# Kernel tuning notes

Hardware: AMD Instinct MI355X
Metric: run time of the kernel (lower is better)

The kernel has to match this reference:

```python
import jax, jax.numpy as jnp
import numpy as np

B, TQ, TP, DQ, DP = 16, 1024, 1024, 1024, 1024

def setup_inputs() -> dict:
    key = jax.random.key(0)
    kq, kp, kw = jax.random.split(key, 3)
    q = jax.random.normal(kq, (B, TQ, DQ), dtype=jnp.float32)
    p = jax.random.normal(kp, (B, TP, DP), dtype=jnp.float32)
    W = jax.random.normal(kw, (DP, DQ), dtype=jnp.float32) / np.sqrt(DP)
    return {"q": q, "p": p, "W": W}

def reference(q, p, W):
    # pW: [B, Tp, Dq]
    pW = jnp.einsum('bpe,ed->bpd', p, W)
    # bilinear scores: [B, Tp, Tq]
    scores = jnp.einsum('bpd,bqd->bpq', pW, q)
    # NOTE: original softmaxes over axis=-2 of [B, Tp, Tq] == the Tp axis
    weights = jax.nn.softmax(scores, axis=1)
    # weighted sum over Tq: [B, Tp, Dq]
    out = jnp.einsum('bpq,bqd->bpd', weights, q)
    return out
```

## Files before the change

kernel.cpp:

```cpp
#include <hip/hip_runtime.h>
#include <cstddef>
#include <cstdint>


namespace {

using u16 = unsigned short;
using frag  = __attribute__((ext_vector_type(8))) short;
using f32x4 = __attribute__((ext_vector_type(4))) float;

constexpr int kB = 16;
constexpr int kT = 1024;
constexpr int kD = 1024;
constexpr int BM = 128, BN = 128, BK = 32;
constexpr int KSTEPS = kD / BK;

union FragU { frag v; u16 u[8]; };

__device__ __forceinline__ u16 f2bf(float x) {
  uint32_t u = __float_as_uint(x);
  return (u16)((u + 0x7FFFu + ((u >> 16) & 1u)) >> 16);
}
__device__ __forceinline__ float bf2f(u16 h) {
  return __uint_as_float(((uint32_t)h) << 16);
}

#define AS1(p) (const __attribute__((address_space(1))) void*)(p)
#define AS3(p) (__attribute__((address_space(3))) void*)(p)

__device__ __forceinline__ void gl_lds16(const u16* g, u16* l) {
  __builtin_amdgcn_global_load_lds(AS1(g), AS3(l), 16, 0, 0);
}

__device__ __forceinline__ void stage_glds(const u16* __restrict__ src, u16* lds,
                                           int row0, int k0, int tid) {
  const int w = tid >> 6, l = tid & 63;
#pragma unroll
  for (int rr = 0; rr < 2; ++rr) {
    const int chunk = rr * 4 + w;
    const int row = chunk * 16 + (l >> 2);
    const int kc = (l & 3) * 8;
    gl_lds16(src + (size_t)(row0 + row) * 1024 + k0 + kc, lds + chunk * 512);
  }
}

struct Reg16 { float4 v[4]; };

__device__ __forceinline__ Reg16 load_tile16(const float* __restrict__ src,
                                             int row0, int k0, int tid) {
  const int r = tid >> 1, c0 = (tid & 1) << 4;
  const float4* g = (const float4*)(src + (size_t)(row0 + r) * 1024 + k0 + c0);
  Reg16 out;
#pragma unroll
  for (int i = 0; i < 4; ++i) out.v[i] = g[i];
  return out;
}

__device__ __forceinline__ void write_split(const Reg16& rg, u16* ldsHi, u16* ldsLo,
                                            int tid) {
  const int r = tid >> 1, c0 = (tid & 1) << 4;
  float vv[16];
#pragma unroll
  for (int i = 0; i < 4; ++i) {
    vv[4*i+0] = rg.v[i].x; vv[4*i+1] = rg.v[i].y;
    vv[4*i+2] = rg.v[i].z; vv[4*i+3] = rg.v[i].w;
  }
  FragU h0, l0, h1, l1;
#pragma unroll
  for (int i = 0; i < 8; ++i) {
    u16 h = f2bf(vv[i]);     h0.u[i] = h; l0.u[i] = f2bf(vv[i]     - bf2f(h));
  }
#pragma unroll
  for (int i = 0; i < 8; ++i) {
    u16 h = f2bf(vv[8+i]);   h1.u[i] = h; l1.u[i] = f2bf(vv[8+i]   - bf2f(h));
  }
  *(frag*)(ldsHi + r*32 + c0)     = h0.v;
  *(frag*)(ldsHi + r*32 + c0 + 8) = h1.v;
  *(frag*)(ldsLo + r*32 + c0)     = l0.v;
  *(frag*)(ldsLo + r*32 + c0 + 8) = l1.v;
}

__device__ __forceinline__ void write_split_exp(const Reg16& rg, const float* mL,
                                                const float* rL, u16* ldsHi,
                                                u16* ldsLo, int k0, int tid) {
  const int r = tid >> 1, c0 = (tid & 1) << 4;
  float vv[16];
#pragma unroll
  for (int i = 0; i < 4; ++i) {
    vv[4*i+0] = rg.v[i].x; vv[4*i+1] = rg.v[i].y;
    vv[4*i+2] = rg.v[i].z; vv[4*i+3] = rg.v[i].w;
  }
#pragma unroll
  for (int i = 0; i < 16; ++i) {
    const int k = k0 + c0 + i;
    vv[i] = __expf(vv[i] - mL[k]) * rL[k];
  }
  FragU h0, l0, h1, l1;
#pragma unroll
  for (int i = 0; i < 8; ++i) {
    u16 h = f2bf(vv[i]);   h0.u[i] = h; l0.u[i] = f2bf(vv[i]   - bf2f(h));
  }
#pragma unroll
  for (int i = 0; i < 8; ++i) {
    u16 h = f2bf(vv[8+i]); h1.u[i] = h; l1.u[i] = f2bf(vv[8+i] - bf2f(h));
  }
  *(frag*)(ldsHi + r*32 + c0)     = h0.v;
  *(frag*)(ldsHi + r*32 + c0 + 8) = h1.v;
  *(frag*)(ldsLo + r*32 + c0)     = l0.v;
  *(frag*)(ldsLo + r*32 + c0 + 8) = l1.v;
}

__device__ __forceinline__ void compute_step(const u16* AhS, const u16* AlS,
                                             const u16* BhS, const u16* BlS,
                                             f32x4 acc[4][4], int lane, int wr, int wc) {
  const int kb = (lane >> 4) * 8;
  const int ra = lane & 15;
  frag ah[4], al[4];
#pragma unroll
  for (int m = 0; m < 4; ++m) {
    const int row = wr*64 + m*16 + ra;
    ah[m] = *(const frag*)(AhS + row*32 + kb);
    al[m] = *(const frag*)(AlS + row*32 + kb);
  }
#pragma unroll
  for (int n = 0; n < 4; ++n) {
    const int col = wc*64 + n*16 + ra;
    const frag bh = *(const frag*)(BhS + col*32 + kb);
    const frag bl = *(const frag*)(BlS + col*32 + kb);
#pragma unroll
    for (int m = 0; m < 4; ++m) {
      acc[m][n] = __builtin_amdgcn_mfma_f32_16x16x32_bf16(ah[m], bh, acc[m][n], 0, 0, 0);
      acc[m][n] = __builtin_amdgcn_mfma_f32_16x16x32_bf16(al[m], bh, acc[m][n], 0, 0, 0);
      acc[m][n] = __builtin_amdgcn_mfma_f32_16x16x32_bf16(ah[m], bl, acc[m][n], 0, 0, 0);
    }
  }
}

__device__ __forceinline__ void epilogue_f32(float* __restrict__ dst, f32x4 acc[4][4],
                                             int row0, int col0, int lane, int wr, int wc) {
#pragma unroll
  for (int m = 0; m < 4; ++m)
#pragma unroll
    for (int n = 0; n < 4; ++n) {
      const int col = col0 + wc*64 + n*16 + (lane & 15);
      const int rb  = row0 + wr*64 + m*16 + ((lane >> 4) << 2);
#pragma unroll
      for (int j = 0; j < 4; ++j)
        dst[(size_t)(rb + j) * 1024 + col] = acc[m][n][j];
    }
}

__global__ __launch_bounds__(256) void g1_pw(const float* __restrict__ P,
                                             const u16* __restrict__ WTh,
                                             const u16* __restrict__ WTl,
                                             u16* __restrict__ pWh,
                                             u16* __restrict__ pWl) {
  __shared__ u16 AhS[BM*BK], AlS[BM*BK], BhS[BN*BK], BlS[BN*BK];
  const int tid = threadIdx.x, lane = tid & 63;
  const int wid = tid >> 6, wr = wid >> 1, wc = wid & 1;
  const int m0 = blockIdx.y * BM, n0 = blockIdx.x * BN;

  f32x4 acc[4][4];
#pragma unroll
  for (int m = 0; m < 4; ++m)
#pragma unroll
    for (int n = 0; n < 4; ++n) acc[m][n] = (f32x4){0.f, 0.f, 0.f, 0.f};

  Reg16 a = load_tile16(P, m0, 0, tid);
#pragma unroll 1
  for (int ks = 0; ks < KSTEPS; ++ks) {
    const int k0 = ks * BK;
    __syncthreads();
    stage_glds(WTh, BhS, n0, k0, tid);
    stage_glds(WTl, BlS, n0, k0, tid);
    write_split(a, AhS, AlS, tid);
    if (ks + 1 < KSTEPS) a = load_tile16(P, m0, k0 + BK, tid);
    __syncthreads();
    compute_step(AhS, AlS, BhS, BlS, acc, lane, wr, wc);
  }

#pragma unroll
  for (int m = 0; m < 4; ++m)
#pragma unroll
    for (int n = 0; n < 4; ++n) {
      const int col = n0 + wc*64 + n*16 + (lane & 15);
      const int rb  = m0 + wr*64 + m*16 + ((lane >> 4) << 2);
#pragma unroll
      for (int j = 0; j < 4; ++j) {
        const float x = acc[m][n][j];
        const u16 h = f2bf(x);
        pWh[(size_t)(rb + j) * 1024 + col] = h;
        pWl[(size_t)(rb + j) * 1024 + col] = f2bf(x - bf2f(h));
      }
    }
}

__global__ __launch_bounds__(256) void g2_scores(const u16* __restrict__ pWh,
                                                 const u16* __restrict__ pWl,
                                                 const float* __restrict__ Q,
                                                 float* __restrict__ S) {
  __shared__ u16 AhS[BM*BK], AlS[BM*BK], BhS[BN*BK], BlS[BN*BK];
  const int tid = threadIdx.x, lane = tid & 63;
  const int wid = tid >> 6, wr = wid >> 1, wc = wid & 1;
  const int b = blockIdx.z;
  const int m0 = blockIdx.y * BM, n0 = blockIdx.x * BN;
  const int rowA0 = b * kT + m0;
  const float* Qb = Q + (size_t)b * kT * kD;
  float* Sb = S + (size_t)b * kT * kT;

  f32x4 acc[4][4];
#pragma unroll
  for (int m = 0; m < 4; ++m)
#pragma unroll
    for (int n = 0; n < 4; ++n) acc[m][n] = (f32x4){0.f, 0.f, 0.f, 0.f};

  Reg16 bq = load_tile16(Qb, n0, 0, tid);
#pragma unroll 1
  for (int ks = 0; ks < KSTEPS; ++ks) {
    const int k0 = ks * BK;
    __syncthreads();
    stage_glds(pWh, AhS, rowA0, k0, tid);
    stage_glds(pWl, AlS, rowA0, k0, tid);
    write_split(bq, BhS, BlS, tid);
    if (ks + 1 < KSTEPS) bq = load_tile16(Qb, n0, k0 + BK, tid);
    __syncthreads();
    compute_step(AhS, AlS, BhS, BlS, acc, lane, wr, wc);
  }
  epilogue_f32(Sb, acc, m0, n0, lane, wr, wc);
}

__global__ __launch_bounds__(256) void k3_stats(const float* __restrict__ S,
                                                float* __restrict__ mOut,
                                                float* __restrict__ rlOut) {
  const int b = blockIdx.y;
  const int q0 = blockIdx.x * 32;
  const int t = threadIdx.x;
  const int c = t & 31, g = t >> 5;
  const float* Sb = S + (size_t)b * kT * kT + q0 + c;

  float m = -3.4e38f, l = 0.f;
#pragma unroll 4
  for (int p = g; p < kT; p += 8) {
    const float x = Sb[(size_t)p * kT];
    if (x <= m) {
      l += __expf(x - m);
    } else {
      l = l * __expf(m - x) + 1.f;
      m = x;
    }
  }
  __shared__ float sm[8][32], sl[8][32];
  sm[g][c] = m;
  sl[g][c] = l;
  __syncthreads();
  if (t < 32) {
    float M = sm[0][t];
#pragma unroll
    for (int g2 = 1; g2 < 8; ++g2) M = fmaxf(M, sm[g2][t]);
    float L = 0.f;
#pragma unroll
    for (int g2 = 0; g2 < 8; ++g2) L += sl[g2][t] * __expf(sm[g2][t] - M);
    mOut[(size_t)b * kT + q0 + t] = M;
    rlOut[(size_t)b * kT + q0 + t] = 1.f / L;
  }
}

__global__ __launch_bounds__(256) void conv_t_split(const float* __restrict__ src,
                                                    u16* __restrict__ dstH,
                                                    u16* __restrict__ dstL) {
  __shared__ float ts[64][65];
  const size_t boff = (size_t)blockIdx.z * kT * kD;
  const int t = threadIdx.x;
  const int i0 = blockIdx.y * 64, j0 = blockIdx.x * 64;
  const int r = t >> 2, c0 = (t & 3) << 4;
  const float4* g = (const float4*)(src + boff + (size_t)(i0 + r) * 1024 + j0 + c0);
#pragma unroll
  for (int i = 0; i < 4; ++i) {
    const float4 v = g[i];
    ts[r][c0 + 4*i + 0] = v.x; ts[r][c0 + 4*i + 1] = v.y;
    ts[r][c0 + 4*i + 2] = v.z; ts[r][c0 + 4*i + 3] = v.w;
  }
  __syncthreads();
  FragU h0, l0, h1, l1;
#pragma unroll
  for (int i = 0; i < 8; ++i) {
    const float x = ts[c0 + i][r];
    const u16 h = f2bf(x); h0.u[i] = h; l0.u[i] = f2bf(x - bf2f(h));
  }
#pragma unroll
  for (int i = 0; i < 8; ++i) {
    const float x = ts[c0 + 8 + i][r];
    const u16 h = f2bf(x); h1.u[i] = h; l1.u[i] = f2bf(x - bf2f(h));
  }
  u16* dh = dstH + boff + (size_t)(j0 + r) * 1024 + i0 + c0;
  u16* dl = dstL + boff + (size_t)(j0 + r) * 1024 + i0 + c0;
  *(frag*)dh = h0.v; *((frag*)dh + 1) = h1.v;
  *(frag*)dl = l0.v; *((frag*)dl + 1) = l1.v;
}

__global__ __launch_bounds__(256) void g4_out(const float* __restrict__ S,
                                              const float* __restrict__ mArr,
                                              const float* __restrict__ rlArr,
                                              const u16* __restrict__ qTh,
                                              const u16* __restrict__ qTl,
                                              float* __restrict__ Out) {
  __shared__ u16 AhS[BM*BK], AlS[BM*BK], BhS[BN*BK], BlS[BN*BK];
  __shared__ float mL[kT], rL[kT];
  const int tid = threadIdx.x, lane = tid & 63;
  const int wid = tid >> 6, wr = wid >> 1, wc = wid & 1;
  const int b = blockIdx.z;
  const int m0 = blockIdx.y * BM, n0 = blockIdx.x * BN;
  const float* Sb = S + (size_t)b * kT * kT;
  const u16* qThb = qTh + (size_t)b * kT * kD;
  const u16* qTlb = qTl + (size_t)b * kT * kD;
  float* Ob = Out + (size_t)b * kT * kD;

  for (int i = tid; i < kT; i += 256) {
    mL[i] = mArr[(size_t)b * kT + i];
    rL[i] = rlArr[(size_t)b * kT + i];
  }

  f32x4 acc[4][4];
#pragma unroll
  for (int m = 0; m < 4; ++m)
#pragma unroll
    for (int n = 0; n < 4; ++n) acc[m][n] = (f32x4){0.f, 0.f, 0.f, 0.f};

  Reg16 a = load_tile16(Sb, m0, 0, tid);
#pragma unroll 1
  for (int ks = 0; ks < KSTEPS; ++ks) {
    const int k0 = ks * BK;
    __syncthreads();
    stage_glds(qThb, BhS, n0, k0, tid);
    stage_glds(qTlb, BlS, n0, k0, tid);
    write_split_exp(a, mL, rL, AhS, AlS, k0, tid);
    if (ks + 1 < KSTEPS) a = load_tile16(Sb, m0, k0 + BK, tid);
    __syncthreads();
    compute_step(AhS, AlS, BhS, BlS, acc, lane, wr, wc);
  }
  epilogue_f32(Ob, acc, m0, n0, lane, wr, wc);
}

}

extern "C" void kernel_launch(void* const* d_in, const int* in_sizes, int n_in,
                              void* d_out, int out_size, void* d_ws, size_t ws_size,
                              hipStream_t stream) {
  const float* q = (const float*)d_in[0];
  const float* p = (const float*)d_in[1];
  const float* W = (const float*)d_in[2];
  float* out = (float*)d_out;

  char* wsb = (char*)d_ws;
  u16* pWh = (u16*)wsb;
  u16* pWl = (u16*)(wsb + (32ull << 20));
  u16* qTh = pWh;
  u16* qTl = pWl;
  float* S   = (float*)(wsb + (64ull << 20));
  u16* WTh = (u16*)(wsb + (64ull << 20));
  u16* WTl = (u16*)(wsb + (64ull << 20) + (2ull << 20));
  float* mArr  = (float*)(wsb + (128ull << 20));
  float* rlArr = mArr + (size_t)kB * kT;

  const dim3 blk(256);
  conv_t_split<<<dim3(16, 16, 1), blk, 0, stream>>>(W, WTh, WTl);
  g1_pw<<<dim3(kD / BN, (kB * kT) / BM), blk, 0, stream>>>(p, WTh, WTl, pWh, pWl);
  g2_scores<<<dim3(kT / BN, kT / BM, kB), blk, 0, stream>>>(pWh, pWl, q, S);
  k3_stats<<<dim3(kT / 32, kB), blk, 0, stream>>>(S, mArr, rlArr);
  conv_t_split<<<dim3(16, 16, kB), blk, 0, stream>>>(q, qTh, qTl);
  g4_out<<<dim3(kD / BN, kT / BM, kB), blk, 0, stream>>>(S, mArr, rlArr, qTh, qTl, out);
}
```

Measured before the change: 613.3 us.

## Store scores transposed, precompute split-bf16 softmax weights, fragment-ordered LDS tiles

Scores are now computed as [q,p] so the softmax over p becomes a contiguous row reduction done by one wave per row. A new kernel applies exp and normalization, transposes the result and writes split-bf16 weights, so the final GEMM stages both operands directly with global-to-LDS loads instead of converting fp32 in registers. LDS tiles switch to an MFMA fragment-ordered layout so each lane reads contiguous 16 bytes. This adds an extra full pass over the score matrix and more workspace traffic in exchange for cheaper strided reductions and simpler GEMM inner loops.

```diff
diff --git a/kernel.cpp b/kernel.cpp
--- a/kernel.cpp
+++ b/kernel.cpp
@@ -32,101 +32,65 @@
   __builtin_amdgcn_global_load_lds(AS1(g), AS3(l), 16, 0, 0);
 }
 
-__device__ __forceinline__ void stage_glds(const u16* __restrict__ src, u16* lds,
-                                           int row0, int k0, int tid) {
+
+__device__ __forceinline__ void stage_frag_glds(const u16* __restrict__ src,
+                                                u16* lds, int row0, int k0, int tid) {
   const int w = tid >> 6, l = tid & 63;
-#pragma unroll
-  for (int rr = 0; rr < 2; ++rr) {
-    const int chunk = rr * 4 + w;
-    const int row = chunk * 16 + (l >> 2);
-    const int kc = (l & 3) * 8;
-    gl_lds16(src + (size_t)(row0 + row) * 1024 + k0 + kc, lds + chunk * 512);
-  }
-}
-
-struct Reg16 { float4 v[4]; };
-
-__device__ __forceinline__ Reg16 load_tile16(const float* __restrict__ src,
-                                             int row0, int k0, int tid) {
-  const int r = tid >> 1, c0 = (tid & 1) << 4;
-  const float4* g = (const float4*)(src + (size_t)(row0 + r) * 1024 + k0 + c0);
-  Reg16 out;
-#pragma unroll
-  for (int i = 0; i < 4; ++i) out.v[i] = g[i];
-  return out;
-}
-
-__device__ __forceinline__ void write_split(const Reg16& rg, u16* ldsHi, u16* ldsLo,
-                                            int tid) {
-  const int r = tid >> 1, c0 = (tid & 1) << 4;
-  float vv[16];
-#pragma unroll
-  for (int i = 0; i < 4; ++i) {
-    vv[4*i+0] = rg.v[i].x; vv[4*i+1] = rg.v[i].y;
-    vv[4*i+2] = rg.v[i].z; vv[4*i+3] = rg.v[i].w;
-  }
-  FragU h0, l0, h1, l1;
-#pragma unroll
-  for (int i = 0; i < 8; ++i) {
-    u16 h = f2bf(vv[i]);     h0.u[i] = h; l0.u[i] = f2bf(vv[i]     - bf2f(h));
-  }
-#pragma unroll
-  for (int i = 0; i < 8; ++i) {
-    u16 h = f2bf(vv[8+i]);   h1.u[i] = h; l1.u[i] = f2bf(vv[8+i]   - bf2f(h));
-  }
-  *(frag*)(ldsHi + r*32 + c0)     = h0.v;
-  *(frag*)(ldsHi + r*32 + c0 + 8) = h1.v;
-  *(frag*)(ldsLo + r*32 + c0)     = l0.v;
-  *(frag*)(ldsLo + r*32 + c0 + 8) = l1.v;
-}
-
-__device__ __forceinline__ void write_split_exp(const Reg16& rg, const float* mL,
-                                                const float* rL, u16* ldsHi,
-                                                u16* ldsLo, int k0, int tid) {
-  const int r = tid >> 1, c0 = (tid & 1) << 4;
-  float vv[16];
-#pragma unroll
-  for (int i = 0; i < 4; ++i) {
-    vv[4*i+0] = rg.v[i].x; vv[4*i+1] = rg.v[i].y;
-    vv[4*i+2] = rg.v[i].z; vv[4*i+3] = rg.v[i].w;
-  }
-#pragma unroll
-  for (int i = 0; i < 16; ++i) {
-    const int k = k0 + c0 + i;
-    vv[i] = __expf(vv[i] - mL[k]) * rL[k];
-  }
-  FragU h0, l0, h1, l1;
-#pragma unroll
-  for (int i = 0; i < 8; ++i) {
-    u16 h = f2bf(vv[i]);   h0.u[i] = h; l0.u[i] = f2bf(vv[i]   - bf2f(h));
-  }
-#pragma unroll
-  for (int i = 0; i < 8; ++i) {
-    u16 h = f2bf(vv[8+i]); h1.u[i] = h; l1.u[i] = f2bf(vv[8+i] - bf2f(h));
-  }
-  *(frag*)(ldsHi + r*32 + c0)     = h0.v;
-  *(frag*)(ldsHi + r*32 + c0 + 8) = h1.v;
-  *(frag*)(ldsLo + r*32 + c0)     = l0.v;
-  *(frag*)(ldsLo + r*32 + c0 + 8) = l1.v;
+  const int rl = l & 15;
+  const int kc = (l >> 4) * 8;
+#pragma unroll
+  for (int i = 0; i < 2; ++i) {
+    const int g = w * 2 + i;
+    gl_lds16(src + (size_t)(row0 + g * 16 + rl) * 1024 + k0 + kc, lds + g * 512);
+  }
+}
+
+__device__ __forceinline__ void load_f32_slots(const float* __restrict__ src,
+                                               int row0, int k0, int tid, float4* out) {
+#pragma unroll
+  for (int i = 0; i < 2; ++i) {
+    const int s = tid + i * 256;
+    const int row = (s >> 6) * 16 + (s & 15);
+    const int kc = ((s >> 4) & 3) * 8;
+    const float4* g = (const float4*)(src + (size_t)(row0 + row) * 1024 + k0 + kc);
+    out[i * 2 + 0] = g[0];
+    out[i * 2 + 1] = g[1];
+  }
+}
+
+__device__ __forceinline__ void write_split_frag(const float4* v, u16* ldsHi,
+                                                 u16* ldsLo, int tid) {
+#pragma unroll
+  for (int i = 0; i < 2; ++i) {
+    const int s = tid + i * 256;
+    const float vv[8] = {v[2*i].x, v[2*i].y, v[2*i].z, v[2*i].w,
+                         v[2*i+1].x, v[2*i+1].y, v[2*i+1].z, v[2*i+1].w};
+    FragU h, lo;
+#pragma unroll
+    for (int j = 0; j < 8; ++j) {
+      const u16 hh = f2bf(vv[j]);
+      h.u[j] = hh;
+      lo.u[j] = f2bf(vv[j] - bf2f(hh));
+    }
+    *(frag*)(ldsHi + s * 8) = h.v;
+    *(frag*)(ldsLo + s * 8) = lo.v;
+  }
 }
 
 __device__ __forceinline__ void compute_step(const u16* AhS, const u16* AlS,
                                              const u16* BhS, const u16* BlS,
                                              f32x4 acc[4][4], int lane, int wr, int wc) {
-  const int kb = (lane >> 4) * 8;
-  const int ra = lane & 15;
+  const int lo16 = lane * 8;
   frag ah[4], al[4];
 #pragma unroll
   for (int m = 0; m < 4; ++m) {
-    const int row = wr*64 + m*16 + ra;
-    ah[m] = *(const frag*)(AhS + row*32 + kb);
-    al[m] = *(const frag*)(AlS + row*32 + kb);
+    ah[m] = *(const frag*)(AhS + (wr * 4 + m) * 512 + lo16);
+    al[m] = *(const frag*)(AlS + (wr * 4 + m) * 512 + lo16);
   }
 #pragma unroll
   for (int n = 0; n < 4; ++n) {
-    const int col = wc*64 + n*16 + ra;
-    const frag bh = *(const frag*)(BhS + col*32 + kb);
-    const frag bl = *(const frag*)(BlS + col*32 + kb);
+    const frag bh = *(const frag*)(BhS + (wc * 4 + n) * 512 + lo16);
+    const frag bl = *(const frag*)(BlS + (wc * 4 + n) * 512 + lo16);
 #pragma unroll
     for (int m = 0; m < 4; ++m) {
       acc[m][n] = __builtin_amdgcn_mfma_f32_16x16x32_bf16(ah[m], bh, acc[m][n], 0, 0, 0);
@@ -142,8 +106,8 @@
   for (int m = 0; m < 4; ++m)
 #pragma unroll
     for (int n = 0; n < 4; ++n) {
-      const int col = col0 + wc*64 + n*16 + (lane & 15);
-      const int rb  = row0 + wr*64 + m*16 + ((lane >> 4) << 2);
+      const int col = col0 + wc * 64 + n * 16 + (lane & 15);
+      const int rb  = row0 + wr * 64 + m * 16 + ((lane >> 4) << 2);
 #pragma unroll
       for (int j = 0; j < 4; ++j)
         dst[(size_t)(rb + j) * 1024 + col] = acc[m][n][j];
@@ -155,7 +119,7 @@
                                              const u16* __restrict__ WTl,
                                              u16* __restrict__ pWh,
                                              u16* __restrict__ pWl) {
-  __shared__ u16 AhS[BM*BK], AlS[BM*BK], BhS[BN*BK], BlS[BN*BK];
+  __shared__ __align__(16) u16 AhS[4096], AlS[4096], BhS[4096], BlS[4096];
   const int tid = threadIdx.x, lane = tid & 63;
   const int wid = tid >> 6, wr = wid >> 1, wc = wid & 1;
   const int m0 = blockIdx.y * BM, n0 = blockIdx.x * BN;
@@ -166,15 +130,16 @@
 #pragma unroll
     for (int n = 0; n < 4; ++n) acc[m][n] = (f32x4){0.f, 0.f, 0.f, 0.f};
 
-  Reg16 a = load_tile16(P, m0, 0, tid);
+  float4 areg[4];
+  load_f32_slots(P, m0, 0, tid, areg);
 #pragma unroll 1
   for (int ks = 0; ks < KSTEPS; ++ks) {
     const int k0 = ks * BK;
     __syncthreads();
-    stage_glds(WTh, BhS, n0, k0, tid);
-    stage_glds(WTl, BlS, n0, k0, tid);
-    write_split(a, AhS, AlS, tid);
-    if (ks + 1 < KSTEPS) a = load_tile16(P, m0, k0 + BK, tid);
+    stage_frag_glds(WTh, BhS, n0, k0, tid);
+    stage_frag_glds(WTl, BlS, n0, k0, tid);
+    write_split_frag(areg, AhS, AlS, tid);
+    if (ks + 1 < KSTEPS) load_f32_slots(P, m0, k0 + BK, tid, areg);
     __syncthreads();
     compute_step(AhS, AlS, BhS, BlS, acc, lane, wr, wc);
   }
@@ -183,8 +148,8 @@
   for (int m = 0; m < 4; ++m)
 #pragma unroll
     for (int n = 0; n < 4; ++n) {
-      const int col = n0 + wc*64 + n*16 + (lane & 15);
-      const int rb  = m0 + wr*64 + m*16 + ((lane >> 4) << 2);
+      const int col = n0 + wc * 64 + n * 16 + (lane & 15);
+      const int rb  = m0 + wr * 64 + m * 16 + ((lane >> 4) << 2);
 #pragma unroll
       for (int j = 0; j < 4; ++j) {
         const float x = acc[m][n][j];
@@ -195,18 +160,18 @@
     }
 }
 
-__global__ __launch_bounds__(256) void g2_scores(const u16* __restrict__ pWh,
-                                                 const u16* __restrict__ pWl,
-                                                 const float* __restrict__ Q,
-                                                 float* __restrict__ S) {
-  __shared__ u16 AhS[BM*BK], AlS[BM*BK], BhS[BN*BK], BlS[BN*BK];
+__global__ __launch_bounds__(256) void g2_scoresT(const float* __restrict__ Q,
+                                                  const u16* __restrict__ pWh,
+                                                  const u16* __restrict__ pWl,
+                                                  float* __restrict__ Sp) {
+  __shared__ __align__(16) u16 AhS[4096], AlS[4096], BhS[4096], BlS[4096];
   const int tid = threadIdx.x, lane = tid & 63;
   const int wid = tid >> 6, wr = wid >> 1, wc = wid & 1;
   const int b = blockIdx.z;
   const int m0 = blockIdx.y * BM, n0 = blockIdx.x * BN;
-  const int rowA0 = b * kT + m0;
   const float* Qb = Q + (size_t)b * kT * kD;
-  float* Sb = S + (size_t)b * kT * kT;
+  const int rowB0 = b * kT + n0;
+  float* Sb = Sp + (size_t)b * kT * kT;
 
   f32x4 acc[4][4];
 #pragma unroll
@@ -214,55 +179,93 @@
 #pragma unroll
     for (int n = 0; n < 4; ++n) acc[m][n] = (f32x4){0.f, 0.f, 0.f, 0.f};
 
-  Reg16 bq = load_tile16(Qb, n0, 0, tid);
+  float4 areg[4];
+  load_f32_slots(Qb, m0, 0, tid, areg);
 #pragma unroll 1
   for (int ks = 0; ks < KSTEPS; ++ks) {
     const int k0 = ks * BK;
     __syncthreads();
-    stage_glds(pWh, AhS, rowA0, k0, tid);
-    stage_glds(pWl, AlS, rowA0, k0, tid);
-    write_split(bq, BhS, BlS, tid);
-    if (ks + 1 < KSTEPS) bq = load_tile16(Qb, n0, k0 + BK, tid);
+    stage_frag_glds(pWh, BhS, rowB0, k0, tid);
+    stage_frag_glds(pWl, BlS, rowB0, k0, tid);
+    write_split_frag(areg, AhS, AlS, tid);
+    if (ks + 1 < KSTEPS) load_f32_slots(Qb, m0, k0 + BK, tid, areg);
     __syncthreads();
     compute_step(AhS, AlS, BhS, BlS, acc, lane, wr, wc);
   }
   epilogue_f32(Sb, acc, m0, n0, lane, wr, wc);
 }
 
-__global__ __launch_bounds__(256) void k3_stats(const float* __restrict__ S,
-                                                float* __restrict__ mOut,
-                                                float* __restrict__ rlOut) {
-  const int b = blockIdx.y;
-  const int q0 = blockIdx.x * 32;
+__global__ __launch_bounds__(256) void k3_rows(const float* __restrict__ Sp,
+                                               float* __restrict__ mOut,
+                                               float* __restrict__ rlOut) {
+  const int row = blockIdx.x * 4 + (threadIdx.x >> 6);
+  const int lane = threadIdx.x & 63;
+  const float4* r = (const float4*)(Sp + (size_t)row * kT);
+
+  float4 v[4];
+#pragma unroll
+  for (int i = 0; i < 4; ++i) v[i] = r[lane + i * 64];
+
+  float m = -3.4e38f;
+#pragma unroll
+  for (int i = 0; i < 4; ++i)
+    m = fmaxf(m, fmaxf(fmaxf(v[i].x, v[i].y), fmaxf(v[i].z, v[i].w)));
+#pragma unroll
+  for (int off = 32; off > 0; off >>= 1) m = fmaxf(m, __shfl_xor(m, off));
+
+  float l = 0.f;
+#pragma unroll
+  for (int i = 0; i < 4; ++i) {
+    l += __expf(v[i].x - m) + __expf(v[i].y - m) +
+         __expf(v[i].z - m) + __expf(v[i].w - m);
+  }
+#pragma unroll
+  for (int off = 32; off > 0; off >>= 1) l += __shfl_xor(l, off);
+
+  if (lane == 0) {
+    mOut[row] = m;
+    rlOut[row] = 1.f / l;
+  }
+}
+
+__global__ __launch_bounds__(256) void k5_expT(const float* __restrict__ Sp,
+                                               const float* __restrict__ mArr,
+                                               const float* __restrict__ rlArr,
+                                               u16* __restrict__ Wh,
+                                               u16* __restrict__ Wl) {
+  __shared__ float ts[64][65];
+  const int b = blockIdx.z;
+  const float* Sb = Sp + (size_t)b * kT * kT;
   const int t = threadIdx.x;
-  const int c = t & 31, g = t >> 5;
-  const float* Sb = S + (size_t)b * kT * kT + q0 + c;
-
-  float m = -3.4e38f, l = 0.f;
-#pragma unroll 4
-  for (int p = g; p < kT; p += 8) {
-    const float x = Sb[(size_t)p * kT];
-    if (x <= m) {
-      l += __expf(x - m);
-    } else {
-      l = l * __expf(m - x) + 1.f;
-      m = x;
-    }
-  }
-  __shared__ float sm[8][32], sl[8][32];
-  sm[g][c] = m;
-  sl[g][c] = l;
+  const int i0 = blockIdx.y * 64, j0 = blockIdx.x * 64;
+  const int r = t >> 2, c0 = (t & 3) << 4;
+  const float mv = mArr[(size_t)b * kT + i0 + r];
+  const float rv = rlArr[(size_t)b * kT + i0 + r];
+  const float4* g = (const float4*)(Sb + (size_t)(i0 + r) * 1024 + j0 + c0);
+#pragma unroll
+  for (int i = 0; i < 4; ++i) {
+    const float4 v = g[i];
+    ts[r][c0 + 4*i + 0] = __expf(v.x - mv) * rv;
+    ts[r][c0 + 4*i + 1] = __expf(v.y - mv) * rv;
+    ts[r][c0 + 4*i + 2] = __expf(v.z - mv) * rv;
+    ts[r][c0 + 4*i + 3] = __expf(v.w - mv) * rv;
+  }
   __syncthreads();
-  if (t < 32) {
-    float M = sm[0][t];
-#pragma unroll
-    for (int g2 = 1; g2 < 8; ++g2) M = fmaxf(M, sm[g2][t]);
-    float L = 0.f;
-#pragma unroll
-    for (int g2 = 0; g2 < 8; ++g2) L += sl[g2][t] * __expf(sm[g2][t] - M);
-    mOut[(size_t)b * kT + q0 + t] = M;
-    rlOut[(size_t)b * kT + q0 + t] = 1.f / L;
-  }
+  FragU h0, l0, h1, l1;
+#pragma unroll
+  for (int i = 0; i < 8; ++i) {
+    const float x = ts[c0 + i][r];
+    const u16 h = f2bf(x); h0.u[i] = h; l0.u[i] = f2bf(x - bf2f(h));
+  }
+#pragma unroll
+  for (int i = 0; i < 8; ++i) {
+    const float x = ts[c0 + 8 + i][r];
+    const u16 h = f2bf(x); h1.u[i] = h; l1.u[i] = f2bf(x - bf2f(h));
+  }
+  u16* dh = Wh + (size_t)b * kT * kT + (size_t)(j0 + r) * 1024 + i0 + c0;
+  u16* dl = Wl + (size_t)b * kT * kT + (size_t)(j0 + r) * 1024 + i0 + c0;
+  *(frag*)dh = h0.v; *((frag*)dh + 1) = h1.v;
+  *(frag*)dl = l0.v; *((frag*)dl + 1) = l1.v;
 }
 
 __global__ __launch_bounds__(256) void conv_t_split(const float* __restrict__ src,
@@ -298,43 +301,35 @@
   *(frag*)dl = l0.v; *((frag*)dl + 1) = l1.v;
 }
 
-__global__ __launch_bounds__(256) void g4_out(const float* __restrict__ S,
-                                              const float* __restrict__ mArr,
-                                              const float* __restrict__ rlArr,
+__global__ __launch_bounds__(256) void g4_out(const u16* __restrict__ Wh,
+                                              const u16* __restrict__ Wl,
                                               const u16* __restrict__ qTh,
                                               const u16* __restrict__ qTl,
                                               float* __restrict__ Out) {
-  __shared__ u16 AhS[BM*BK], AlS[BM*BK], BhS[BN*BK], BlS[BN*BK];
-  __shared__ float mL[kT], rL[kT];
+  __shared__ __align__(16) u16 AhS[4096], AlS[4096], BhS[4096], BlS[4096];
   const int tid = threadIdx.x, lane = tid & 63;
   const int wid = tid >> 6, wr = wid >> 1, wc = wid & 1;
   const int b = blockIdx.z;
   const int m0 = blockIdx.y * BM, n0 = blockIdx.x * BN;
-  const float* Sb = S + (size_t)b * kT * kT;
-  const u16* qThb = qTh + (size_t)b * kT * kD;
-  const u16* qTlb = qTl + (size_t)b * kT * kD;
+  const int rowA0 = b * kT + m0;
+  const u16* qThb = qTh + (size_t)b * kD * kT;
+  const u16* qTlb = qTl + (size_t)b * kD * kT;
   float* Ob = Out + (size_t)b * kT * kD;
 
-  for (int i = tid; i < kT; i += 256) {
-    mL[i] = mArr[(size_t)b * kT + i];
-    rL[i] = rlArr[(size_t)b * kT + i];
-  }
-
   f32x4 acc[4][4];
 #pragma unroll
   for (int m = 0; m < 4; ++m)
 #pragma unroll
     for (int n = 0; n < 4; ++n) acc[m][n] = (f32x4){0.f, 0.f, 0.f, 0.f};
 
-  Reg16 a = load_tile16(Sb, m0, 0, tid);
 #pragma unroll 1
   for (int ks = 0; ks < KSTEPS; ++ks) {
     const int k0 = ks * BK;
     __syncthreads();
-    stage_glds(qThb, BhS, n0, k0, tid);
-    stage_glds(qTlb, BlS, n0, k0, tid);
-    write_split_exp(a, mL, rL, AhS, AlS, k0, tid);
-    if (ks + 1 < KSTEPS) a = load_tile16(Sb, m0, k0 + BK, tid);
+    stage_frag_glds(Wh, AhS, rowA0, k0, tid);
+    stage_frag_glds(Wl, AlS, rowA0, k0, tid);
+    stage_frag_glds(qThb, BhS, n0, k0, tid);
+    stage_frag_glds(qTlb, BlS, n0, k0, tid);
     __syncthreads();
     compute_step(AhS, AlS, BhS, BlS, acc, lane, wr, wc);
   }
@@ -354,19 +349,22 @@
   char* wsb = (char*)d_ws;
   u16* pWh = (u16*)wsb;
   u16* pWl = (u16*)(wsb + (32ull << 20));
-  u16* qTh = pWh;
-  u16* qTl = pWl;
-  float* S   = (float*)(wsb + (64ull << 20));
+  u16* Wsh = pWh;
+  u16* Wsl = pWl;
+  float* Sp  = (float*)(wsb + (64ull << 20));
   u16* WTh = (u16*)(wsb + (64ull << 20));
   u16* WTl = (u16*)(wsb + (64ull << 20) + (2ull << 20));
+  u16* qTh = (u16*)(wsb + (64ull << 20));
+  u16* qTl = (u16*)(wsb + (96ull << 20));
   float* mArr  = (float*)(wsb + (128ull << 20));
   float* rlArr = mArr + (size_t)kB * kT;
 
   const dim3 blk(256);
   conv_t_split<<<dim3(16, 16, 1), blk, 0, stream>>>(W, WTh, WTl);
   g1_pw<<<dim3(kD / BN, (kB * kT) / BM), blk, 0, stream>>>(p, WTh, WTl, pWh, pWl);
-  g2_scores<<<dim3(kT / BN, kT / BM, kB), blk, 0, stream>>>(pWh, pWl, q, S);
-  k3_stats<<<dim3(kT / 32, kB), blk, 0, stream>>>(S, mArr, rlArr);
+  g2_scoresT<<<dim3(kT / BN, kT / BM, kB), blk, 0, stream>>>(q, pWh, pWl, Sp);
+  k3_rows<<<dim3((kB * kT) / 4), blk, 0, stream>>>(Sp, mArr, rlArr);
+  k5_expT<<<dim3(16, 16, kB), blk, 0, stream>>>(Sp, mArr, rlArr, Wsh, Wsl);
   conv_t_split<<<dim3(16, 16, kB), blk, 0, stream>>>(q, qTh, qTl);
-  g4_out<<<dim3(kD / BN, kT / BM, kB), blk, 0, stream>>>(S, mArr, rlArr, qTh, qTl, out);
-}
+  g4_out<<<dim3(kD / BN, kT / BM, kB), blk, 0, stream>>>(Wsh, Wsl, qTh, qTl, out);
+}
```

New measurement: 665.2 us. 8.5% more time.
